# Kernel tuning notes

Measured on AMD Instinct MI355X. Metric: run time of the kernel, lower is better.

Reference implementation:

```python
import jax, jax.numpy as jnp
import numpy as np

NEG_SLOPE = 0.2  # PyG GATConv leaky_relu slope


def _gat_layer(x, src, dst, W, a_src, a_dst, b, concat, num_nodes):
    # x: [N, F_in], W: [F_in, H*C], a_src/a_dst: [H, C], b: [H*C] or [C]
    H, C = a_src.shape
    h = (x @ W).reshape(num_nodes, H, C)                      # [N, H, C]
    s_src = jnp.einsum('nhc,hc->nh', h, a_src)                # [N, H]
    s_dst = jnp.einsum('nhc,hc->nh', h, a_dst)                # [N, H]
    e = jax.nn.leaky_relu(s_src[src] + s_dst[dst], NEG_SLOPE) # [E, H]
    # segment softmax over edges sharing a destination node
    m = jax.ops.segment_max(e, dst, num_segments=num_nodes)
    m = jnp.where(jnp.isfinite(m), m, 0.0)
    p = jnp.exp(e - m[dst])
    z = jax.ops.segment_sum(p, dst, num_segments=num_nodes)
    alpha = p / (z[dst] + 1e-16)                              # [E, H]
    msg = h[src] * alpha[:, :, None]                          # [E, H, C]
    out = jax.ops.segment_sum(msg, dst, num_segments=num_nodes)  # [N, H, C]
    out = out.reshape(num_nodes, H * C) if concat else out.mean(axis=1)
    return out + b


def setup_inputs() -> dict:
    key = jax.random.key(0)
    ks = jax.random.split(key, 16)
    N, E, F = 100000, 800000, 128
    H, C = 4, 32
    sc_in = 1.0 / np.sqrt(F)
    inp = {
        'x': jax.random.normal(ks[0], (N, F), jnp.float32),
        'edge_index': jax.random.randint(ks[1], (2, E), 0, N, jnp.int64),
        'W1': jax.random.normal(ks[2], (F, H * C), jnp.float32) * sc_in,
        'a_src1': jax.random.normal(ks[3], (H, C), jnp.float32),
        'a_dst1': jax.random.normal(ks[4], (H, C), jnp.float32),
        'b1': jax.random.normal(ks[5], (H * C,), jnp.float32) * 0.01,
        'W2': jax.random.normal(ks[6], (F, H * C), jnp.float32) * sc_in,
        'a_src2': jax.random.normal(ks[7], (H, C), jnp.float32),
        'a_dst2': jax.random.normal(ks[8], (H, C), jnp.float32),
        'b2': jax.random.normal(ks[9], (H * C,), jnp.float32) * 0.01,
        'W3': jax.random.normal(ks[10], (F, H * F), jnp.float32) * sc_in,
        'a_src3': jax.random.normal(ks[11], (H, F), jnp.float32),
        'a_dst3': jax.random.normal(ks[12], (H, F), jnp.float32),
        'b3': jax.random.normal(ks[13], (F,), jnp.float32) * 0.01,
    }
    return inp


def reference(x, edge_index, W1, a_src1, a_dst1, b1, W2, a_src2, a_dst2, b2,
              W3, a_src3, a_dst3, b3):
    N = x.shape[0]
    # PyG GATConv default: add self loops
    loop = jnp.arange(N, dtype=edge_index.dtype)
    src = jnp.concatenate([edge_index[0], loop])
    dst = jnp.concatenate([edge_index[1], loop])
    # conv1 (concat heads) + residual + ELU
    x1 = jax.nn.elu(_gat_layer(x, src, dst, W1, a_src1, a_dst1, b1, True, N) + x)
    # intermediate conv (concat heads) + residual + ELU
    x2 = jax.nn.elu(_gat_layer(x1, src, dst, W2, a_src2, a_dst2, b2, True, N) + x1)
    # final conv (mean over heads) + residual, no ELU
    x3 = _gat_layer(x2, src, dst, W3, a_src3, a_dst3, b3, False, N) + x2
    return x3
```

## Files before the change

kernel.cpp:

```cpp
#include <hip/hip_runtime.h>
#include <hip/hip_bf16.h>
#include <cstdint>

#define NEG_SLOPE 0.2f

typedef __bf16 bf16x8 __attribute__((ext_vector_type(8)));
typedef _Float16 half8 __attribute__((ext_vector_type(8)));
typedef float  floatx4 __attribute__((ext_vector_type(4)));

__device__ __forceinline__ float us2f(unsigned short u) {
    union { unsigned int i; float f; } c; c.i = ((unsigned int)u) << 16; return c.f;
}
__device__ __forceinline__ unsigned short f2us(float f) {
    union { float f; unsigned int i; } c; c.f = f;
    unsigned int x = c.i;
    unsigned int r = (x + 0x7fffu + ((x >> 16) & 1u)) >> 16;
    return (unsigned short)r;
}
__device__ __forceinline__ unsigned short f2h(float f) {
    union { _Float16 h; unsigned short u; } c; c.h = (_Float16)f; return c.u;
}
__device__ __forceinline__ float h2f(unsigned short u) {
    union { _Float16 h; unsigned short u; } c; c.u = u; return (float)c.h;
}
__device__ __forceinline__ float ldx(const void* p, int i, int bf) {
    return bf ? us2f(((const unsigned short*)p)[i]) : ((const float*)p)[i];
}
__device__ __forceinline__ void split2(float f, unsigned short& h, unsigned short& l) {
    h = f2us(f);
    l = f2us(f - us2f(h));
}
__device__ __forceinline__ float sel4(const float* a, int i) {
    float lo = (i & 1) ? a[1] : a[0];
    float hi = (i & 1) ? a[3] : a[2];
    return (i & 2) ? hi : lo;
}
__device__ __forceinline__ void unp8(uint4 u, float* f) {
    union { unsigned int i; float ff; } a;
    a.i = u.x << 16;          f[0] = a.ff;
    a.i = u.x & 0xffff0000u;  f[1] = a.ff;
    a.i = u.y << 16;          f[2] = a.ff;
    a.i = u.y & 0xffff0000u;  f[3] = a.ff;
    a.i = u.z << 16;          f[4] = a.ff;
    a.i = u.z & 0xffff0000u;  f[5] = a.ff;
    a.i = u.w << 16;          f[6] = a.ff;
    a.i = u.w & 0xffff0000u;  f[7] = a.ff;
}

__global__ void k_detect(const unsigned short* __restrict__ x16,
                         const unsigned int* __restrict__ ei,
                         int* __restrict__ flags) {
    if (threadIdx.x == 0 && blockIdx.x == 0) {
        int cnt = 0;
        for (int i = 0; i < 1024; ++i) {
            const unsigned short u = x16[2 * i];
            const int e = (u >> 7) & 0xFF;
            if (e < 100 || e > 160) ++cnt;
        }
        flags[0] = (cnt < 256) ? 1 : 0;
        int is64 = 1;
        for (int i = 0; i < 64; ++i)
            if (ei[2 * i + 1] != 0u) { is64 = 0; break; }
        flags[1] = is64;
    }
}

__device__ __forceinline__ int edge_at(const void* ei, int f64, long long idx) {
    if (f64) return (int)((const long long*)ei)[idx];
    return ((const int*)ei)[idx];
}

__global__ void k_hist(const void* __restrict__ ei, const int* __restrict__ flags,
                       int* __restrict__ deg, int E, int N) {
    const int f64 = flags[1];
    const int EP = E + N;
    for (int e = blockIdx.x * blockDim.x + threadIdx.x; e < EP; e += gridDim.x * blockDim.x) {
        int dst = (e < E) ? edge_at(ei, f64, (long long)E + e) : (e - E);
        atomicAdd(&deg[dst], 1);
    }
}

__global__ __launch_bounds__(1024) void k_scan_a(const int* __restrict__ deg,
                                                 int* __restrict__ coff,
                                                 int* __restrict__ part, int N) {
    __shared__ int tmp[1024];
    const int t = threadIdx.x, idx = blockIdx.x * 1024 + t;
    const int v = (idx < N) ? deg[idx] : 0;
    tmp[t] = v; __syncthreads();
    for (int s = 1; s < 1024; s <<= 1) {
        int a = (t >= s) ? tmp[t - s] : 0;
        __syncthreads(); tmp[t] += a; __syncthreads();
    }
    if (idx < N) coff[idx] = tmp[t] - v;
    if (t == 1023) part[blockIdx.x] = tmp[1023];
}

__global__ __launch_bounds__(1024) void k_scan_b(int* __restrict__ part,
                                                 int* __restrict__ coff, int nblk, int N) {
    __shared__ int tmp[1024];
    const int t = threadIdx.x;
    const int v = (t < nblk) ? part[t] : 0;
    tmp[t] = v; __syncthreads();
    for (int s = 1; s < 1024; s <<= 1) {
        int a = (t >= s) ? tmp[t - s] : 0;
        __syncthreads(); tmp[t] += a; __syncthreads();
    }
    if (t < nblk) part[t] = tmp[t] - v;
    if (t == 1023) coff[N] = tmp[1023];
}

__global__ __launch_bounds__(1024) void k_scan_c(int* __restrict__ coff,
                                                 const int* __restrict__ part, int N) {
    const int idx = blockIdx.x * 1024 + threadIdx.x;
    if (idx < N) coff[idx] += part[blockIdx.x];
}

__global__ void k_scatter(const void* __restrict__ ei, const int* __restrict__ flags,
                          const int* __restrict__ coff, int* __restrict__ cpos,
                          int* __restrict__ csrc, int E, int N) {
    const int f64 = flags[1];
    const int EP = E + N;
    for (int e = blockIdx.x * blockDim.x + threadIdx.x; e < EP; e += gridDim.x * blockDim.x) {
        int src, dst;
        if (e < E) { src = edge_at(ei, f64, e); dst = edge_at(ei, f64, (long long)E + e); }
        else       { src = dst = e - E; }
        const int p = atomicAdd(&cpos[dst], 1);
        csrc[coff[dst] + p] = src;
    }
}

template <int F16>
__global__ void k_wfrag(const void* __restrict__ Wv, const int* __restrict__ flags,
                        int wstride, int total,
                        unsigned short* __restrict__ outH, unsigned short* __restrict__ outL) {
    const int bf = flags[0];
    for (int tid = blockIdx.x * blockDim.x + threadIdx.x; tid < total;
         tid += gridDim.x * blockDim.x) {
        const int j    = tid & 7;
        const int lane = (tid >> 3) & 63;
        const int ks   = (tid >> 9) & 3;
        const int ntg  = (tid >> 11) & 7;
        const int blk  = tid >> 14;
        const int k = ks * 32 + (lane >> 4) * 8 + j;
        const int c = blk * 128 + ntg * 16 + (lane & 15);
        const float v = ldx(Wv, k * wstride + c, bf);
        unsigned short h, l;
        if (F16) {
            h = f2h(v);
            l = f2h(v - h2f(h));
        } else {
            split2(v, h, l);
        }
        outH[tid] = h; outL[tid] = l;
    }
}

__global__ void k_wa(const void* __restrict__ W, const void* __restrict__ as,
                     const void* __restrict__ ad, const int* __restrict__ flags,
                     float* __restrict__ va) {
    const int bf = flags[0];
    const int t = blockIdx.x * blockDim.x + threadIdx.x;
    if (t >= 512) return;
    const int k = t >> 2, h = t & 3;
    float ss = 0.f, dd = 0.f;
    for (int c = 0; c < 128; ++c) {
        const float w = ldx(W, k * 512 + h * 128 + c, bf);
        ss = fmaf(w, ldx(as, h * 128 + c, bf), ss);
        dd = fmaf(w, ldx(ad, h * 128 + c, bf), dd);
    }
    va[k * 8 + h] = ss;
    va[k * 8 + 4 + h] = dd;
}

template <bool XRAW, int SC>
__global__ __launch_bounds__(256) void k_gemm(const void* __restrict__ Xv,
                                              const unsigned short* __restrict__ whfB,
                                              const unsigned short* __restrict__ wlfB,
                                              unsigned short* __restrict__ Y16, int ystride,
                                              float* __restrict__ ssrc,
                                              float* __restrict__ sdst,
                                              const void* __restrict__ a_src,
                                              const void* __restrict__ a_dst,
                                              const int* __restrict__ flags,
                                              int N) {
    __shared__ __align__(16) unsigned short Ah[64][136], Al[64][136];
    __shared__ float sred[2][4][SC ? 64 : 1];
    const int bf   = flags[0];
    const int t    = threadIdx.x;
    const int row0 = blockIdx.x * 64;
    const int hy   = blockIdx.y;
    const unsigned short* whf = whfB + hy * 16384;
    const unsigned short* wlf = wlfB + hy * 16384;
    const int ycol0 = hy * 128;
    const int wv   = t >> 6;
    const int lane = t & 63;
    const int quad = lane >> 4;
    const int l16  = lane & 15;

#pragma unroll
    for (int it = 0; it < 8; ++it) {
        const int id = it * 256 + t;
        const int r  = id >> 5;
        const int c  = (id & 31) * 4;
        const int gr = row0 + r;
        ushort4 h4 = make_ushort4(0, 0, 0, 0), l4 = make_ushort4(0, 0, 0, 0);
        if (gr < N) {
            if (XRAW && bf) {
                h4 = *(const ushort4*)&((const unsigned short*)Xv)[(size_t)gr * 128 + c];
            } else {
                const float4 f = *(const float4*)&((const float*)Xv)[(size_t)gr * 128 + c];
                split2(f.x, h4.x, l4.x); split2(f.y, h4.y, l4.y);
                split2(f.z, h4.z, l4.z); split2(f.w, h4.w, l4.w);
            }
        }
        *(ushort4*)&Ah[r][c] = h4;
        *(ushort4*)&Al[r][c] = l4;
    }
    __syncthreads();

    floatx4 acc[4][2];
#pragma unroll
    for (int mt = 0; mt < 4; ++mt)
#pragma unroll
        for (int nt = 0; nt < 2; ++nt) acc[mt][nt] = (floatx4){0.f, 0.f, 0.f, 0.f};

#pragma unroll
    for (int ks = 0; ks < 4; ++ks) {
        const int ko = ks * 32 + quad * 8;
        bf16x8 ah[4], al[4], bh[2], bl[2];
#pragma unroll
        for (int mt = 0; mt < 4; ++mt) ah[mt] = *(const bf16x8*)&Ah[mt * 16 + l16][ko];
        if (!(XRAW && bf)) {
#pragma unroll
            for (int mt = 0; mt < 4; ++mt) al[mt] = *(const bf16x8*)&Al[mt * 16 + l16][ko];
        }
#pragma unroll
        for (int nt = 0; nt < 2; ++nt)
            bh[nt] = *(const bf16x8*)&whf[(((wv * 2 + nt) * 4 + ks) * 64 + lane) * 8];
        if (!bf) {
#pragma unroll
            for (int nt = 0; nt < 2; ++nt)
                bl[nt] = *(const bf16x8*)&wlf[(((wv * 2 + nt) * 4 + ks) * 64 + lane) * 8];
        }
#pragma unroll
        for (int mt = 0; mt < 4; ++mt)
#pragma unroll
            for (int nt = 0; nt < 2; ++nt) {
                acc[mt][nt] = __builtin_amdgcn_mfma_f32_16x16x32_bf16(ah[mt], bh[nt], acc[mt][nt], 0, 0, 0);
                if (!bf)
                    acc[mt][nt] = __builtin_amdgcn_mfma_f32_16x16x32_bf16(ah[mt], bl[nt], acc[mt][nt], 0, 0, 0);
                if (!(XRAW && bf))
                    acc[mt][nt] = __builtin_amdgcn_mfma_f32_16x16x32_bf16(al[mt], bh[nt], acc[mt][nt], 0, 0, 0);
            }
    }

    const int aBase = hy * 128 + wv * 32;
    float as_[2], ad_[2];
#pragma unroll
    for (int nt = 0; nt < 2; ++nt) {
        as_[nt] = ldx(a_src, aBase + nt * 16 + l16, bf);
        ad_[nt] = ldx(a_dst, aBase + nt * 16 + l16, bf);
    }

#pragma unroll
    for (int mt = 0; mt < 4; ++mt) {
        const int rl = mt * 16 + quad * 4;
#pragma unroll
        for (int r = 0; r < 4; ++r) {
            const int grow = row0 + rl + r;
            if (grow < N) {
#pragma unroll
                for (int nt = 0; nt < 2; ++nt)
                    Y16[(size_t)grow * ystride + ycol0 + wv * 32 + nt * 16 + l16] =
                        f2us(acc[mt][nt][r]);
            }
            float ps = acc[mt][0][r] * as_[0] + acc[mt][1][r] * as_[1];
            float pd = acc[mt][0][r] * ad_[0] + acc[mt][1][r] * ad_[1];
#pragma unroll
            for (int mk = 1; mk <= 8; mk <<= 1) {
                ps += __shfl_xor(ps, mk);
                pd += __shfl_xor(pd, mk);
            }
            if (SC == 0) {
                if (l16 == 0 && grow < N) {
                    ssrc[(size_t)grow * 4 + wv] = ps;
                    sdst[(size_t)grow * 4 + wv] = pd;
                }
            } else {
                if (l16 == 0) { sred[0][wv][rl + r] = ps; sred[1][wv][rl + r] = pd; }
            }
        }
    }
    if (SC == 1) {
        __syncthreads();
        if (t < 64 && row0 + t < N) {
            ssrc[(size_t)(row0 + t) * 4 + hy] = sred[0][0][t] + sred[0][1][t] + sred[0][2][t] + sred[0][3][t];
            sdst[(size_t)(row0 + t) * 4 + hy] = sred[1][0][t] + sred[1][1][t] + sred[1][2][t] + sred[1][3][t];
        }
    }
}

template <int MODE>
__global__ __launch_bounds__(256) void k_agg(const int* __restrict__ coff,
                                             const int* __restrict__ csrc,
                                             const float* __restrict__ ssrc,
                                             const float* __restrict__ sdst,
                                             const unsigned short* __restrict__ H16,
                                             const void* __restrict__ bias,
                                             const void* __restrict__ resid,
                                             const int* __restrict__ flags,
                                             void* __restrict__ out, int N,
                                             const float* __restrict__ va,
                                             float* __restrict__ ss2,
                                             float* __restrict__ sd2,
                                             unsigned short* __restrict__ x2h,
                                             unsigned short* __restrict__ x2l) {
    __shared__ float vaS[(MODE == 1) ? 128 : 1][10];
    const int bf   = flags[0];
    const int t    = threadIdx.x;
    const int l16  = t & 15;
    const int n0   = blockIdx.x * 16 + (t >> 4);
    const bool nact = n0 < N;
    const int n    = nact ? n0 : (N - 1);
    const int beg = coff[n], end = coff[n + 1];
    const int deg = end - beg;

    if (MODE == 1) {
        for (int i = t; i < 1024; i += 256) vaS[i >> 3][i & 7] = va[i];
        __syncthreads();
    }

    const float4 sdv = *(const float4*)&sdst[(size_t)n * 4];
    const float sd[4] = { sdv.x, sdv.y, sdv.z, sdv.w };
    const bool fast = (deg <= 16);
    float z[4];
    int   myS = 0;
    float wn[4] = { 0.f, 0.f, 0.f, 0.f };

    if (fast) {
        const bool act = l16 < deg;
        if (act) {
            myS = csrc[beg + l16];
            const float4 sp = *(const float4*)&ssrc[(size_t)myS * 4];
            const float s4[4] = { sp.x, sp.y, sp.z, sp.w };
#pragma unroll
            for (int h = 0; h < 4; ++h) {
                float tv = s4[h] + sd[h];
                tv = tv >= 0.f ? tv : NEG_SLOPE * tv;
                wn[h] = __expf(fminf(tv, 80.f));
            }
        }
#pragma unroll
        for (int h = 0; h < 4; ++h) z[h] = wn[h];
#pragma unroll
        for (int mk = 1; mk <= 8; mk <<= 1)
#pragma unroll
            for (int h = 0; h < 4; ++h) z[h] += __shfl_xor(z[h], mk);
    } else {
#pragma unroll
        for (int h = 0; h < 4; ++h) z[h] = 0.f;
        for (int e = beg + l16; e < end; e += 16) {
            const int s = csrc[e];
            const float4 sp = *(const float4*)&ssrc[(size_t)s * 4];
            const float s4[4] = { sp.x, sp.y, sp.z, sp.w };
#pragma unroll
            for (int h = 0; h < 4; ++h) {
                float tv = s4[h] + sd[h];
                tv = tv >= 0.f ? tv : NEG_SLOPE * tv;
                z[h] += __expf(fminf(tv, 80.f));
            }
        }
#pragma unroll
        for (int mk = 1; mk <= 8; mk <<= 1)
#pragma unroll
            for (int h = 0; h < 4; ++h) z[h] += __shfl_xor(z[h], mk);
    }

    float ivz[4];
#pragma unroll
    for (int h = 0; h < 4; ++h) ivz[h] = 1.f / (z[h] + 1e-16f);

    const int c8 = l16 * 8;
    const int hd = l16 >> 2;
    const float ih = sel4(ivz, hd);
    float ac[8];
#pragma unroll
    for (int j = 0; j < 8; ++j) ac[j] = 0.f;

    if (fast) {
        for (int e = 0; e < deg; ++e) {
            const int s = __shfl(myS, e, 16);
            float wa4[4];
            wa4[0] = __shfl(wn[0], e, 16);
            wa4[1] = __shfl(wn[1], e, 16);
            wa4[2] = __shfl(wn[2], e, 16);
            wa4[3] = __shfl(wn[3], e, 16);
            const float w = sel4(wa4, hd);
            const uint4 u = *(const uint4*)&H16[(size_t)s * 128 + c8];
            float f[8]; unp8(u, f);
#pragma unroll
            for (int j = 0; j < 8; ++j) ac[j] = fmaf(w, f[j], ac[j]);
        }
    } else {
        const float sdh = sel4(sd, hd);
        for (int e = beg; e < end; ++e) {
            const int s = csrc[e];
            float tv = ssrc[(size_t)s * 4 + hd] + sdh;
            tv = tv >= 0.f ? tv : NEG_SLOPE * tv;
            const float w = __expf(fminf(tv, 80.f));
            const uint4 u = *(const uint4*)&H16[(size_t)s * 128 + c8];
            float f[8]; unp8(u, f);
#pragma unroll
            for (int j = 0; j < 8; ++j) ac[j] = fmaf(w, f[j], ac[j]);
        }
    }

#pragma unroll
    for (int j = 0; j < 8; ++j) ac[j] *= ih;

    if (!nact) return;
    const int ob = n * 128 + c8;
    float rr[8];
    if (MODE == 0) {
        if (bf) {
            const uint4 u = *(const uint4*)&((const unsigned short*)resid)[ob];
            unp8(u, rr);
        } else {
            const float4 r0 = *(const float4*)&((const float*)resid)[ob];
            const float4 r1 = *(const float4*)&((const float*)resid)[ob + 4];
            rr[0] = r0.x; rr[1] = r0.y; rr[2] = r0.z; rr[3] = r0.w;
            rr[4] = r1.x; rr[5] = r1.y; rr[6] = r1.z; rr[7] = r1.w;
        }
    } else {
        const float4 r0 = *(const float4*)&((const float*)resid)[ob];
        const float4 r1 = *(const float4*)&((const float*)resid)[ob + 4];
        rr[0] = r0.x; rr[1] = r0.y; rr[2] = r0.z; rr[3] = r0.w;
        rr[4] = r1.x; rr[5] = r1.y; rr[6] = r1.z; rr[7] = r1.w;
    }
    float o[8];
#pragma unroll
    for (int j = 0; j < 8; ++j) {
        const float v = ac[j] + ldx(bias, c8 + j, bf) + rr[j];
        o[j] = v > 0.f ? v : expm1f(v);
    }
    if (MODE == 0) {
        *(float4*)&((float*)out)[ob]     = make_float4(o[0], o[1], o[2], o[3]);
        *(float4*)&((float*)out)[ob + 4] = make_float4(o[4], o[5], o[6], o[7]);
    }

    if (MODE == 1) {
        unsigned short hi[8], lo[8];
#pragma unroll
        for (int j = 0; j < 8; ++j) {
            hi[j] = f2us(o[j]);
            lo[j] = f2us(o[j] - us2f(hi[j]));
        }
        uint4 uh, ul;
        uh.x = (unsigned int)hi[0] | ((unsigned int)hi[1] << 16);
        uh.y = (unsigned int)hi[2] | ((unsigned int)hi[3] << 16);
        uh.z = (unsigned int)hi[4] | ((unsigned int)hi[5] << 16);
        uh.w = (unsigned int)hi[6] | ((unsigned int)hi[7] << 16);
        ul.x = (unsigned int)lo[0] | ((unsigned int)lo[1] << 16);
        ul.y = (unsigned int)lo[2] | ((unsigned int)lo[3] << 16);
        ul.z = (unsigned int)lo[4] | ((unsigned int)lo[5] << 16);
        ul.w = (unsigned int)lo[6] | ((unsigned int)lo[7] << 16);
        *(uint4*)&x2h[ob] = uh;
        *(uint4*)&x2l[ob] = ul;
        float p[8];
#pragma unroll
        for (int o8 = 0; o8 < 8; ++o8) {
            float acc = 0.f;
#pragma unroll
            for (int j = 0; j < 8; ++j) acc = fmaf(o[j], vaS[c8 + j][o8], acc);
            p[o8] = acc;
        }
#pragma unroll
        for (int mk = 1; mk <= 8; mk <<= 1)
#pragma unroll
            for (int o8 = 0; o8 < 8; ++o8) p[o8] += __shfl_xor(p[o8], mk);
        if (l16 == 0) {
#pragma unroll
            for (int h = 0; h < 4; ++h) {
                ss2[(size_t)n * 4 + h] = p[h];
                sd2[(size_t)n * 4 + h] = p[4 + h];
            }
        }
    }
}

__global__ __launch_bounds__(256) void k_aggx3(const int* __restrict__ coff,
                                               const int* __restrict__ csrc,
                                               const float* __restrict__ ssrc,
                                               const float* __restrict__ sdst,
                                               const unsigned short* __restrict__ X16,
                                               const unsigned short* __restrict__ Xl16,
                                               const unsigned short* __restrict__ whf,
                                               const void* __restrict__ bias,
                                               const int* __restrict__ flags,
                                               void* __restrict__ out, int N) {
    __shared__ __align__(16) unsigned short aggS[4][16][136];
    const int bf   = flags[0];
    const int t    = threadIdx.x;
    const int row0 = blockIdx.x * 16;
    const int l16  = t & 15;

    {
        const int r  = t >> 4;
        const int n0 = row0 + r;
        const int n  = (n0 < N) ? n0 : (N - 1);
        const int beg = coff[n], end = coff[n + 1];
        const int deg = end - beg;

        const float4 sdv = *(const float4*)&sdst[(size_t)n * 4];
        const float sd[4] = { sdv.x, sdv.y, sdv.z, sdv.w };
        const bool fast = (deg <= 16);
        float m[4], z[4];
        int   myS = 0;
        float wn[4] = { 0.f, 0.f, 0.f, 0.f };

        if (fast) {
            const bool act = l16 < deg;
            float v[4];
#pragma unroll
            for (int h = 0; h < 4; ++h) v[h] = -1e30f;
            if (act) {
                myS = csrc[beg + l16];
                const float4 sp = *(const float4*)&ssrc[(size_t)myS * 4];
                const float s4[4] = { sp.x, sp.y, sp.z, sp.w };
#pragma unroll
                for (int h = 0; h < 4; ++h) {
                    float tv = s4[h] + sd[h];
                    v[h] = tv >= 0.f ? tv : NEG_SLOPE * tv;
                }
            }
#pragma unroll
            for (int h = 0; h < 4; ++h) m[h] = v[h];
#pragma unroll
            for (int mk = 1; mk <= 8; mk <<= 1)
#pragma unroll
                for (int h = 0; h < 4; ++h) m[h] = fmaxf(m[h], __shfl_xor(m[h], mk));
            float w[4];
#pragma unroll
            for (int h = 0; h < 4; ++h) w[h] = act ? __expf(v[h] - m[h]) : 0.f;
#pragma unroll
            for (int h = 0; h < 4; ++h) z[h] = w[h];
#pragma unroll
            for (int mk = 1; mk <= 8; mk <<= 1)
#pragma unroll
                for (int h = 0; h < 4; ++h) z[h] += __shfl_xor(z[h], mk);
#pragma unroll
            for (int h = 0; h < 4; ++h) wn[h] = w[h] / (z[h] + 1e-16f);
        } else {
#pragma unroll
            for (int h = 0; h < 4; ++h) m[h] = -1e30f;
            for (int e = beg + l16; e < end; e += 16) {
                const int s = csrc[e];
                const float4 sp = *(const float4*)&ssrc[(size_t)s * 4];
                const float s4[4] = { sp.x, sp.y, sp.z, sp.w };
#pragma unroll
                for (int h = 0; h < 4; ++h) {
                    float tv = s4[h] + sd[h];
                    tv = tv >= 0.f ? tv : NEG_SLOPE * tv;
                    m[h] = fmaxf(m[h], tv);
                }
            }
#pragma unroll
            for (int mk = 1; mk <= 8; mk <<= 1)
#pragma unroll
                for (int h = 0; h < 4; ++h) m[h] = fmaxf(m[h], __shfl_xor(m[h], mk));
#pragma unroll
            for (int h = 0; h < 4; ++h) z[h] = 0.f;
            for (int e = beg + l16; e < end; e += 16) {
                const int s = csrc[e];
                const float4 sp = *(const float4*)&ssrc[(size_t)s * 4];
                const float s4[4] = { sp.x, sp.y, sp.z, sp.w };
#pragma unroll
                for (int h = 0; h < 4; ++h) {
                    float tv = s4[h] + sd[h];
                    tv = tv >= 0.f ? tv : NEG_SLOPE * tv;
                    z[h] += __expf(tv - m[h]);
                }
            }
#pragma unroll
            for (int mk = 1; mk <= 8; mk <<= 1)
#pragma unroll
                for (int h = 0; h < 4; ++h) z[h] += __shfl_xor(z[h], mk);
        }

        const int c8 = l16 * 8;
        float ac[4][8];
#pragma unroll
        for (int h = 0; h < 4; ++h)
#pragma unroll
            for (int j = 0; j < 8; ++j) ac[h][j] = 0.f;

        if (fast) {
            int e = 0;
            for (; e + 2 <= deg; e += 2) {
                const int s0 = __shfl(myS, e + 0, 16);
                const int s1 = __shfl(myS, e + 1, 16);
                const uint4 u0 = *(const uint4*)&X16[(size_t)s0 * 128 + c8];
                const uint4 u1 = *(const uint4*)&X16[(size_t)s1 * 128 + c8];
                float w0[4], w1[4];
#pragma unroll
                for (int h = 0; h < 4; ++h) {
                    w0[h] = __shfl(wn[h], e + 0, 16);
                    w1[h] = __shfl(wn[h], e + 1, 16);
                }
                float f[8];
                unp8(u0, f);
#pragma unroll
                for (int h = 0; h < 4; ++h)
#pragma unroll
                    for (int j = 0; j < 8; ++j) ac[h][j] = fmaf(w0[h], f[j], ac[h][j]);
                unp8(u1, f);
#pragma unroll
                for (int h = 0; h < 4; ++h)
#pragma unroll
                    for (int j = 0; j < 8; ++j) ac[h][j] = fmaf(w1[h], f[j], ac[h][j]);
            }
            for (; e < deg; ++e) {
                const int s = __shfl(myS, e, 16);
                float wr[4];
                wr[0] = __shfl(wn[0], e, 16);
                wr[1] = __shfl(wn[1], e, 16);
                wr[2] = __shfl(wn[2], e, 16);
                wr[3] = __shfl(wn[3], e, 16);
                const uint4 u = *(const uint4*)&X16[(size_t)s * 128 + c8];
                float f[8]; unp8(u, f);
#pragma unroll
                for (int h = 0; h < 4; ++h)
#pragma unroll
                    for (int j = 0; j < 8; ++j) ac[h][j] = fmaf(wr[h], f[j], ac[h][j]);
            }
        } else {
            float ivh[4];
#pragma unroll
            for (int h = 0; h < 4; ++h) ivh[h] = 1.f / (z[h] + 1e-16f);
            for (int e = beg; e < end; ++e) {
                const int s = csrc[e];
                const float4 sp = *(const float4*)&ssrc[(size_t)s * 4];
                const float s4[4] = { sp.x, sp.y, sp.z, sp.w };
                float wr[4];
#pragma unroll
                for (int h = 0; h < 4; ++h) {
                    float tv = s4[h] + sd[h];
                    tv = tv >= 0.f ? tv : NEG_SLOPE * tv;
                    wr[h] = __expf(tv - m[h]) * ivh[h];
                }
                const uint4 u = *(const uint4*)&X16[(size_t)s * 128 + c8];
                float f[8]; unp8(u, f);
#pragma unroll
                for (int h = 0; h < 4; ++h)
#pragma unroll
                    for (int j = 0; j < 8; ++j) ac[h][j] = fmaf(wr[h], f[j], ac[h][j]);
            }
        }

#pragma unroll
        for (int h = 0; h < 4; ++h) {
            uint4 u;
            u.x = (unsigned int)f2h(ac[h][0]) | ((unsigned int)f2h(ac[h][1]) << 16);
            u.y = (unsigned int)f2h(ac[h][2]) | ((unsigned int)f2h(ac[h][3]) << 16);
            u.z = (unsigned int)f2h(ac[h][4]) | ((unsigned int)f2h(ac[h][5]) << 16);
            u.w = (unsigned int)f2h(ac[h][6]) | ((unsigned int)f2h(ac[h][7]) << 16);
            *(uint4*)&aggS[h][r][c8] = u;
        }
    }
    __syncthreads();

    const int wv   = t >> 6;
    const int lane = t & 63;
    const int quad = lane >> 4;
    const int q16  = lane & 15;

    floatx4 acc[2];
#pragma unroll
    for (int nt = 0; nt < 2; ++nt) acc[nt] = (floatx4){0.f, 0.f, 0.f, 0.f};

#pragma unroll
    for (int kc = 0; kc < 4; ++kc) {
        const unsigned short* whc = whf + kc * 16384;
#pragma unroll
        for (int ks = 0; ks < 4; ++ks) {
            const int ko = ks * 32 + quad * 8;
            half8 ah, bh[2];
            ah = *(const half8*)&aggS[kc][q16][ko];
#pragma unroll
            for (int nt = 0; nt < 2; ++nt)
                bh[nt] = *(const half8*)&whc[(((wv * 2 + nt) * 4 + ks) * 64 + lane) * 8];
#pragma unroll
            for (int nt = 0; nt < 2; ++nt)
                acc[nt] = __builtin_amdgcn_mfma_f32_16x16x32_f16(ah, bh[nt], acc[nt], 0, 0, 0);
        }
    }

    const int rl = quad * 4;
#pragma unroll
    for (int r = 0; r < 4; ++r) {
        const int grow = row0 + rl + r;
        if (grow < N) {
#pragma unroll
            for (int nt = 0; nt < 2; ++nt) {
                const int col = wv * 32 + nt * 16 + q16;
                const size_t ix = (size_t)grow * 128 + col;
                const float resid = us2f(X16[ix]) + us2f(Xl16[ix]);
                const float v = acc[nt][r] * 0.25f + ldx(bias, col, bf) + resid;
                if (bf) ((unsigned short*)out)[ix] = f2us(v);
                else    ((float*)out)[ix] = v;
            }
        }
    }
}

extern "C" void kernel_launch(void* const* d_in, const int* in_sizes, int n_in,
                              void* d_out, int out_size, void* d_ws, size_t ws_size,
                              hipStream_t stream) {
    const int N  = in_sizes[0] / 128;
    const int E  = in_sizes[1] / 2;
    const int EP = E + N;

    const void* x   = d_in[0];
    const void* ei  = d_in[1];
    const void* W1  = d_in[2];
    const void* as1 = d_in[3];
    const void* ad1 = d_in[4];
    const void* b1  = d_in[5];
    const void* W2  = d_in[6];
    const void* as2 = d_in[7];
    const void* ad2 = d_in[8];
    const void* b2  = d_in[9];
    const void* W3  = d_in[10];
    const void* as3 = d_in[11];
    const void* ad3 = d_in[12];
    const void* b3  = d_in[13];

    char* p = (char*)d_ws;
    auto alloc = [&](size_t bytes) { char* r = p; p += (bytes + 255) & ~(size_t)255; return r; };
    int*   flags = (int*)alloc(8);
    int*   deg   = (int*)alloc((size_t)(N + 1) * 4);
    int*   coff  = (int*)alloc((size_t)(N + 1) * 4);
    int*   cpos  = (int*)alloc((size_t)N * 4);
    int*   part  = (int*)alloc(4096);
    int*   csrc  = (int*)alloc((size_t)EP * 4);
    float* x1b   = (float*)alloc((size_t)N * 128 * 4);
    unsigned short* h16_12 = (unsigned short*)alloc((size_t)N * 128 * 2);
    float* ssrc  = (float*)alloc((size_t)N * 4 * 4);
    float* sdst  = (float*)alloc((size_t)N * 4 * 4);
    unsigned short* whf1 = (unsigned short*)alloc(16384 * 2);
    unsigned short* wlf1 = (unsigned short*)alloc(16384 * 2);
    unsigned short* whf2 = (unsigned short*)alloc(16384 * 2);
    unsigned short* wlf2 = (unsigned short*)alloc(16384 * 2);
    unsigned short* whf3 = (unsigned short*)alloc(65536 * 2);
    unsigned short* wlf3 = (unsigned short*)alloc(65536 * 2);
    unsigned short* x2h  = (unsigned short*)alloc((size_t)N * 128 * 2);
    unsigned short* x2l  = (unsigned short*)alloc((size_t)N * 128 * 2);
    float* va    = (float*)alloc(128 * 8 * 4);
    float* ssrc3 = (float*)alloc((size_t)N * 4 * 4);
    float* sdst3 = (float*)alloc((size_t)N * 4 * 4);

    hipMemsetAsync(deg,  0, (size_t)(N + 1) * 4, stream);
    hipMemsetAsync(cpos, 0, (size_t)N * 4, stream);

    k_detect<<<1, 64, 0, stream>>>((const unsigned short*)x, (const unsigned int*)ei, flags);

    k_wfrag<0><<<64, 256, 0, stream>>>(W1, flags, 128, 16384, whf1, wlf1);
    k_wfrag<0><<<64, 256, 0, stream>>>(W2, flags, 128, 16384, whf2, wlf2);
    k_wfrag<1><<<256, 256, 0, stream>>>(W3, flags, 512, 65536, whf3, wlf3);
    k_wa<<<2, 256, 0, stream>>>(W3, as3, ad3, flags, va);

    const int egrid = (EP + 255) / 256;
    const int nblk  = (N + 1023) / 1024;
    k_hist<<<egrid, 256, 0, stream>>>(ei, flags, deg, E, N);
    k_scan_a<<<nblk, 1024, 0, stream>>>(deg, coff, part, N);
    k_scan_b<<<1, 1024, 0, stream>>>(part, coff, nblk, N);
    k_scan_c<<<nblk, 1024, 0, stream>>>(coff, part, N);
    k_scatter<<<egrid, 256, 0, stream>>>(ei, flags, coff, cpos, csrc, E, N);

    const int ggrid = (N + 63) / 64;
    const int ngrid = (N + 15) / 16;

    k_gemm<true, 0><<<dim3(ggrid, 1), 256, 0, stream>>>(x, whf1, wlf1, h16_12, 128,
                                                        ssrc, sdst, as1, ad1, flags, N);
    k_agg<0><<<ngrid, 256, 0, stream>>>(coff, csrc, ssrc, sdst, h16_12, b1, x, flags, x1b, N,
                                        nullptr, nullptr, nullptr, nullptr, nullptr);

    k_gemm<false, 0><<<dim3(ggrid, 1), 256, 0, stream>>>(x1b, whf2, wlf2, h16_12, 128,
                                                         ssrc, sdst, as2, ad2, flags, N);
    k_agg<1><<<ngrid, 256, 0, stream>>>(coff, csrc, ssrc, sdst, h16_12, b2, x1b, flags, nullptr, N,
                                        va, ssrc3, sdst3, x2h, x2l);

    k_aggx3<<<ngrid, 256, 0, stream>>>(coff, csrc, ssrc3, sdst3, x2h, x2l,
                                       whf3, b3, flags, d_out, N);
}
```

Before: 610.7 us.

## Fold attention score projections into GEMM via precomputed W·a MFMA fragments

```diff
diff --git a/kernel.cpp b/kernel.cpp
--- a/kernel.cpp
+++ b/kernel.cpp
@@ -155,6 +155,30 @@
     }
 }
 
+__global__ void k_vaf(const void* __restrict__ W, const void* __restrict__ as,
+                      const void* __restrict__ ad, const int* __restrict__ flags,
+                      unsigned short* __restrict__ outH, unsigned short* __restrict__ outL) {
+    const int bf = flags[0];
+    const int tid = blockIdx.x * blockDim.x + threadIdx.x;
+    if (tid >= 8192) return;
+    const int j    = tid & 7;
+    const int lane = (tid >> 3) & 63;
+    const int ks   = (tid >> 9) & 3;
+    const int head = (tid >> 11) & 3;
+    const int k    = ks * 32 + (lane >> 4) * 8 + j;
+    const int col  = lane & 15;
+    float v = 0.f;
+    if (col < 2) {
+        const void* a = col ? ad : as;
+        float acc = 0.f;
+        for (int c = 0; c < 32; ++c)
+            acc = fmaf(ldx(W, k * 128 + head * 32 + c, bf), ldx(a, head * 32 + c, bf), acc);
+        v = acc;
+    }
+    unsigned short h, l; split2(v, h, l);
+    outH[tid] = h; outL[tid] = l;
+}
+
 __global__ void k_wa(const void* __restrict__ W, const void* __restrict__ as,
                      const void* __restrict__ ad, const int* __restrict__ flags,
                      float* __restrict__ va) {
@@ -172,26 +196,22 @@
     va[k * 8 + 4 + h] = dd;
 }
 
-template <bool XRAW, int SC>
+template <int AM>
 __global__ __launch_bounds__(256) void k_gemm(const void* __restrict__ Xv,
-                                              const unsigned short* __restrict__ whfB,
-                                              const unsigned short* __restrict__ wlfB,
-                                              unsigned short* __restrict__ Y16, int ystride,
+                                              const void* __restrict__ Xlv,
+                                              const unsigned short* __restrict__ whf,
+                                              const unsigned short* __restrict__ wlf,
+                                              const unsigned short* __restrict__ vfh,
+                                              const unsigned short* __restrict__ vfl,
+                                              unsigned short* __restrict__ Y16,
                                               float* __restrict__ ssrc,
                                               float* __restrict__ sdst,
-                                              const void* __restrict__ a_src,
-                                              const void* __restrict__ a_dst,
                                               const int* __restrict__ flags,
                                               int N) {
     __shared__ __align__(16) unsigned short Ah[64][136], Al[64][136];
-    __shared__ float sred[2][4][SC ? 64 : 1];
     const int bf   = flags[0];
     const int t    = threadIdx.x;
     const int row0 = blockIdx.x * 64;
-    const int hy   = blockIdx.y;
-    const unsigned short* whf = whfB + hy * 16384;
-    const unsigned short* wlf = wlfB + hy * 16384;
-    const int ycol0 = hy * 128;
     const int wv   = t >> 6;
     const int lane = t & 63;
     const int quad = lane >> 4;
@@ -205,7 +225,10 @@
         const int gr = row0 + r;
         ushort4 h4 = make_ushort4(0, 0, 0, 0), l4 = make_ushort4(0, 0, 0, 0);
         if (gr < N) {
-            if (XRAW && bf) {
+            if (AM == 1) {
+                h4 = *(const ushort4*)&((const unsigned short*)Xv)[(size_t)gr * 128 + c];
+                l4 = *(const ushort4*)&((const unsigned short*)Xlv)[(size_t)gr * 128 + c];
+            } else if (bf) {
                 h4 = *(const ushort4*)&((const unsigned short*)Xv)[(size_t)gr * 128 + c];
             } else {
                 const float4 f = *(const float4*)&((const float*)Xv)[(size_t)gr * 128 + c];
@@ -219,18 +242,22 @@
     __syncthreads();
 
     floatx4 acc[4][2];
-#pragma unroll
-    for (int mt = 0; mt < 4; ++mt)
+    floatx4 accS[4];
+#pragma unroll
+    for (int mt = 0; mt < 4; ++mt) {
+        accS[mt] = (floatx4){0.f, 0.f, 0.f, 0.f};
 #pragma unroll
         for (int nt = 0; nt < 2; ++nt) acc[mt][nt] = (floatx4){0.f, 0.f, 0.f, 0.f};
+    }
 
 #pragma unroll
     for (int ks = 0; ks < 4; ++ks) {
         const int ko = ks * 32 + quad * 8;
-        bf16x8 ah[4], al[4], bh[2], bl[2];
+        const bool useAl = (AM == 1) || !bf;
+        bf16x8 ah[4], al[4], bh[2], bl[2], vh, vl;
 #pragma unroll
         for (int mt = 0; mt < 4; ++mt) ah[mt] = *(const bf16x8*)&Ah[mt * 16 + l16][ko];
-        if (!(XRAW && bf)) {
+        if (useAl) {
 #pragma unroll
             for (int mt = 0; mt < 4; ++mt) al[mt] = *(const bf16x8*)&Al[mt * 16 + l16][ko];
         }
@@ -242,24 +269,24 @@
             for (int nt = 0; nt < 2; ++nt)
                 bl[nt] = *(const bf16x8*)&wlf[(((wv * 2 + nt) * 4 + ks) * 64 + lane) * 8];
         }
-#pragma unroll
-        for (int mt = 0; mt < 4; ++mt)
+        vh = *(const bf16x8*)&vfh[((wv * 4 + ks) * 64 + lane) * 8];
+        vl = *(const bf16x8*)&vfl[((wv * 4 + ks) * 64 + lane) * 8];
+
+#pragma unroll
+        for (int mt = 0; mt < 4; ++mt) {
 #pragma unroll
             for (int nt = 0; nt < 2; ++nt) {
                 acc[mt][nt] = __builtin_amdgcn_mfma_f32_16x16x32_bf16(ah[mt], bh[nt], acc[mt][nt], 0, 0, 0);
                 if (!bf)
                     acc[mt][nt] = __builtin_amdgcn_mfma_f32_16x16x32_bf16(ah[mt], bl[nt], acc[mt][nt], 0, 0, 0);
-                if (!(XRAW && bf))
+                if ((AM == 1) || !bf)
                     acc[mt][nt] = __builtin_amdgcn_mfma_f32_16x16x32_bf16(al[mt], bh[nt], acc[mt][nt], 0, 0, 0);
             }
-    }
-
-    const int aBase = hy * 128 + wv * 32;
-    float as_[2], ad_[2];
-#pragma unroll
-    for (int nt = 0; nt < 2; ++nt) {
-        as_[nt] = ldx(a_src, aBase + nt * 16 + l16, bf);
-        ad_[nt] = ldx(a_dst, aBase + nt * 16 + l16, bf);
+            accS[mt] = __builtin_amdgcn_mfma_f32_16x16x32_bf16(ah[mt], vh, accS[mt], 0, 0, 0);
+            accS[mt] = __builtin_amdgcn_mfma_f32_16x16x32_bf16(ah[mt], vl, accS[mt], 0, 0, 0);
+            if ((AM == 1) || !bf)
+                accS[mt] = __builtin_amdgcn_mfma_f32_16x16x32_bf16(al[mt], vh, accS[mt], 0, 0, 0);
+        }
     }
 
 #pragma unroll
@@ -271,31 +298,11 @@
             if (grow < N) {
 #pragma unroll
                 for (int nt = 0; nt < 2; ++nt)
-                    Y16[(size_t)grow * ystride + ycol0 + wv * 32 + nt * 16 + l16] =
+                    Y16[(size_t)grow * 128 + wv * 32 + nt * 16 + l16] =
                         f2us(acc[mt][nt][r]);
-            }
-            float ps = acc[mt][0][r] * as_[0] + acc[mt][1][r] * as_[1];
-            float pd = acc[mt][0][r] * ad_[0] + acc[mt][1][r] * ad_[1];
-#pragma unroll
-            for (int mk = 1; mk <= 8; mk <<= 1) {
-                ps += __shfl_xor(ps, mk);
-                pd += __shfl_xor(pd, mk);
-            }
-            if (SC == 0) {
-                if (l16 == 0 && grow < N) {
-                    ssrc[(size_t)grow * 4 + wv] = ps;
-                    sdst[(size_t)grow * 4 + wv] = pd;
-                }
-            } else {
-                if (l16 == 0) { sred[0][wv][rl + r] = ps; sred[1][wv][rl + r] = pd; }
-            }
-        }
-    }
-    if (SC == 1) {
-        __syncthreads();
-        if (t < 64 && row0 + t < N) {
-            ssrc[(size_t)(row0 + t) * 4 + hy] = sred[0][0][t] + sred[0][1][t] + sred[0][2][t] + sred[0][3][t];
-            sdst[(size_t)(row0 + t) * 4 + hy] = sred[1][0][t] + sred[1][1][t] + sred[1][2][t] + sred[1][3][t];
+                if (l16 == 0)      ssrc[(size_t)grow * 4 + wv] = accS[mt][r];
+                else if (l16 == 1) sdst[(size_t)grow * 4 + wv] = accS[mt][r];
+            }
         }
     }
 }
@@ -308,13 +315,14 @@
                                              const unsigned short* __restrict__ H16,
                                              const void* __restrict__ bias,
                                              const void* __restrict__ resid,
+                                             const unsigned short* __restrict__ residL,
                                              const int* __restrict__ flags,
-                                             void* __restrict__ out, int N,
+                                             int N,
                                              const float* __restrict__ va,
                                              float* __restrict__ ss2,
                                              float* __restrict__ sd2,
-                                             unsigned short* __restrict__ x2h,
-                                             unsigned short* __restrict__ x2l) {
+                                             unsigned short* __restrict__ outH,
+                                             unsigned short* __restrict__ outL) {
     __shared__ float vaS[(MODE == 1) ? 128 : 1][10];
     const int bf   = flags[0];
     const int t    = threadIdx.x;
@@ -432,10 +440,11 @@
             rr[4] = r1.x; rr[5] = r1.y; rr[6] = r1.z; rr[7] = r1.w;
         }
     } else {
-        const float4 r0 = *(const float4*)&((const float*)resid)[ob];
-        const float4 r1 = *(const float4*)&((const float*)resid)[ob + 4];
-        rr[0] = r0.x; rr[1] = r0.y; rr[2] = r0.z; rr[3] = r0.w;
-        rr[4] = r1.x; rr[5] = r1.y; rr[6] = r1.z; rr[7] = r1.w;
+        const uint4 uh = *(const uint4*)&((const unsigned short*)resid)[ob];
+        const uint4 ul = *(const uint4*)&residL[ob];
+        float fh[8], fl[8]; unp8(uh, fh); unp8(ul, fl);
+#pragma unroll
+        for (int j = 0; j < 8; ++j) rr[j] = fh[j] + fl[j];
     }
     float o[8];
 #pragma unroll
@@ -443,29 +452,26 @@
         const float v = ac[j] + ldx(bias, c8 + j, bf) + rr[j];
         o[j] = v > 0.f ? v : expm1f(v);
     }
-    if (MODE == 0) {
-        *(float4*)&((float*)out)[ob]     = make_float4(o[0], o[1], o[2], o[3]);
-        *(float4*)&((float*)out)[ob + 4] = make_float4(o[4], o[5], o[6], o[7]);
-    }
+
+    unsigned short hi[8], lo[8];
+#pragma unroll
+    for (int j = 0; j < 8; ++j) {
+        hi[j] = f2us(o[j]);
+        lo[j] = f2us(o[j] - us2f(hi[j]));
+    }
+    uint4 uh, ul;
+    uh.x = (unsigned int)hi[0] | ((unsigned int)hi[1] << 16);
+    uh.y = (unsigned int)hi[2] | ((unsigned int)hi[3] << 16);
+    uh.z = (unsigned int)hi[4] | ((unsigned int)hi[5] << 16);
+    uh.w = (unsigned int)hi[6] | ((unsigned int)hi[7] << 16);
+    ul.x = (unsigned int)lo[0] | ((unsigned int)lo[1] << 16);
+    ul.y = (unsigned int)lo[2] | ((unsigned int)lo[3] << 16);
+    ul.z = (unsigned int)lo[4] | ((unsigned int)lo[5] << 16);
+    ul.w = (unsigned int)lo[6] | ((unsigned int)lo[7] << 16);
+    *(uint4*)&outH[ob] = uh;
+    *(uint4*)&outL[ob] = ul;
 
     if (MODE == 1) {
-        unsigned short hi[8], lo[8];
-#pragma unroll
-        for (int j = 0; j < 8; ++j) {
-            hi[j] = f2us(o[j]);
-            lo[j] = f2us(o[j] - us2f(hi[j]));
-        }
-        uint4 uh, ul;
-        uh.x = (unsigned int)hi[0] | ((unsigned int)hi[1] << 16);
-        uh.y = (unsigned int)hi[2] | ((unsigned int)hi[3] << 16);
-        uh.z = (unsigned int)hi[4] | ((unsigned int)hi[5] << 16);
-        uh.w = (unsigned int)hi[6] | ((unsigned int)hi[7] << 16);
-        ul.x = (unsigned int)lo[0] | ((unsigned int)lo[1] << 16);
-        ul.y = (unsigned int)lo[2] | ((unsigned int)lo[3] << 16);
-        ul.z = (unsigned int)lo[4] | ((unsigned int)lo[5] << 16);
-        ul.w = (unsigned int)lo[6] | ((unsigned int)lo[7] << 16);
-        *(uint4*)&x2h[ob] = uh;
-        *(uint4*)&x2l[ob] = ul;
         float p[8];
 #pragma unroll
         for (int o8 = 0; o8 < 8; ++o8) {
@@ -743,7 +749,8 @@
     int*   cpos  = (int*)alloc((size_t)N * 4);
     int*   part  = (int*)alloc(4096);
     int*   csrc  = (int*)alloc((size_t)EP * 4);
-    float* x1b   = (float*)alloc((size_t)N * 128 * 4);
+    unsigned short* x1h = (unsigned short*)alloc((size_t)N * 128 * 2);
+    unsigned short* x1l = (unsigned short*)alloc((size_t)N * 128 * 2);
     unsigned short* h16_12 = (unsigned short*)alloc((size_t)N * 128 * 2);
     float* ssrc  = (float*)alloc((size_t)N * 4 * 4);
     float* sdst  = (float*)alloc((size_t)N * 4 * 4);
@@ -753,6 +760,10 @@
     unsigned short* wlf2 = (unsigned short*)alloc(16384 * 2);
     unsigned short* whf3 = (unsigned short*)alloc(65536 * 2);
     unsigned short* wlf3 = (unsigned short*)alloc(65536 * 2);
+    unsigned short* vaf1h = (unsigned short*)alloc(8192 * 2);
+    unsigned short* vaf1l = (unsigned short*)alloc(8192 * 2);
+    unsigned short* vaf2h = (unsigned short*)alloc(8192 * 2);
+    unsigned short* vaf2l = (unsigned short*)alloc(8192 * 2);
     unsigned short* x2h  = (unsigned short*)alloc((size_t)N * 128 * 2);
     unsigned short* x2l  = (unsigned short*)alloc((size_t)N * 128 * 2);
     float* va    = (float*)alloc(128 * 8 * 4);
@@ -767,6 +778,8 @@
     k_wfrag<0><<<64, 256, 0, stream>>>(W1, flags, 128, 16384, whf1, wlf1);
     k_wfrag<0><<<64, 256, 0, stream>>>(W2, flags, 128, 16384, whf2, wlf2);
     k_wfrag<1><<<256, 256, 0, stream>>>(W3, flags, 512, 65536, whf3, wlf3);
+    k_vaf<<<32, 256, 0, stream>>>(W1, as1, ad1, flags, vaf1h, vaf1l);
+    k_vaf<<<32, 256, 0, stream>>>(W2, as2, ad2, flags, vaf2h, vaf2l);
     k_wa<<<2, 256, 0, stream>>>(W3, as3, ad3, flags, va);
 
     const int egrid = (EP + 255) / 256;
@@ -780,15 +793,15 @@
     const int ggrid = (N + 63) / 64;
     const int ngrid = (N + 15) / 16;
 
-    k_gemm<true, 0><<<dim3(ggrid, 1), 256, 0, stream>>>(x, whf1, wlf1, h16_12, 128,
-                                                        ssrc, sdst, as1, ad1, flags, N);
-    k_agg<0><<<ngrid, 256, 0, stream>>>(coff, csrc, ssrc, sdst, h16_12, b1, x, flags, x1b, N,
-                                        nullptr, nullptr, nullptr, nullptr, nullptr);
-
-    k_gemm<false, 0><<<dim3(ggrid, 1), 256, 0, stream>>>(x1b, whf2, wlf2, h16_12, 128,
-                                                         ssrc, sdst, as2, ad2, flags, N);
-    k_agg<1><<<ngrid, 256, 0, stream>>>(coff, csrc, ssrc, sdst, h16_12, b2, x1b, flags, nullptr, N,
-                                        va, ssrc3, sdst3, x2h, x2l);
+    k_gemm<0><<<ggrid, 256, 0, stream>>>(x, nullptr, whf1, wlf1, vaf1h, vaf1l,
+                                         h16_12, ssrc, sdst, flags, N);
+    k_agg<0><<<ngrid, 256, 0, stream>>>(coff, csrc, ssrc, sdst, h16_12, b1, x, nullptr,
+                                        flags, N, nullptr, nullptr, nullptr, x1h, x1l);
+
+    k_gemm<1><<<ggrid, 256, 0, stream>>>(x1h, x1l, whf2, wlf2, vaf2h, vaf2l,
+                                         h16_12, ssrc, sdst, flags, N);
+    k_agg<1><<<ngrid, 256, 0, stream>>>(coff, csrc, ssrc, sdst, h16_12, b2, x1h, x1l,
+                                        flags, N, va, ssrc3, sdst3, x2h, x2l);
 
     k_aggx3<<<ngrid, 256, 0, stream>>>(coff, csrc, ssrc3, sdst3, x2h, x2l,
                                        whf3, b3, flags, d_out, N);
```

New measurement: 633.2 us. 3.7% more time.
